# Performance work log

Measured on AMD Instinct MI355X. Metric: run time of the kernel, lower is better.

The kernel has to match this reference:

```python
import jax, jax.numpy as jnp
import numpy as np

DIM = 4096
N_HEADS = 32
N_KV_HEADS = 8
HEAD_DIM = 128
WINDOW = 4096
BATCH = 32
START_POS = 4095


def setup_inputs() -> dict:
    key = jax.random.key(0)
    ks = jax.random.split(key, 8)
    x = jax.random.normal(ks[0], (BATCH, DIM), dtype=jnp.float32)
    wqkv = jax.random.normal(ks[1], (DIM, (N_HEADS + 2 * N_KV_HEADS) * HEAD_DIM), dtype=jnp.float32) * 0.02
    wo = jax.random.normal(ks[2], (N_HEADS * HEAD_DIM, DIM), dtype=jnp.float32) * 0.02
    cos = jax.random.uniform(ks[3], (HEAD_DIM,), dtype=jnp.float32)
    sin = jax.random.uniform(ks[4], (HEAD_DIM,), dtype=jnp.float32)
    cache_k = jax.random.normal(ks[5], (BATCH, N_KV_HEADS, WINDOW, HEAD_DIM), dtype=jnp.float32)
    cache_v = jax.random.normal(ks[6], (BATCH, N_KV_HEADS, WINDOW, HEAD_DIM), dtype=jnp.float32)
    mask = jnp.zeros((BATCH, 1, 1, WINDOW), dtype=jnp.float32)
    return {"x": x, "wqkv": wqkv, "wo": wo, "cos": cos, "sin": sin,
            "cache_k": cache_k, "cache_v": cache_v, "mask": mask,
            "start_pos": START_POS}


def _rotate_half(t):
    t1, t2 = jnp.split(t, 2, axis=-1)
    return jnp.concatenate([-t2, t1], axis=-1)


def _rope(t, cos, sin):
    # t: [..., head_dim]; cos/sin: [head_dim] at the current decode position
    return t * cos + _rotate_half(t) * sin


def reference(x, wqkv, wo, cos, sin, cache_k, cache_v, mask, start_pos):
    B, D = x.shape
    KV = cache_k.shape[1]
    Hd = cache_k.shape[3]
    window = cache_k.shape[2]
    H = wo.shape[0] // Hd
    R = H // KV  # GQA repeats
    scale = 1.0 / np.sqrt(Hd)

    # fused QKV projection (matmul_1d + nlp_create_qkv_heads)
    qkv = x @ wqkv  # [B, (H+2*KV)*Hd]
    q = qkv[:, : H * Hd].reshape(B, H, Hd)
    k = qkv[:, H * Hd : (H + KV) * Hd].reshape(B, KV, Hd)
    v = qkv[:, (H + KV) * Hd :].reshape(B, KV, Hd)

    # rotary embedding on q and k at current position
    q = _rope(q, cos, sin)
    k = _rope(k, cos, sin)

    # sliding-window KV cache update at current_pos
    cur = start_pos % window  # python int
    cache_k = cache_k.at[:, :, cur].set(k)
    cache_v = cache_v.at[:, :, cur].set(v)

    # unpad to padded_layer_past_len = min(nearest_32(start_pos+1), window)
    padded_len = min(((start_pos + 1 + 31) // 32) * 32, window)
    keys = cache_k[:, :, :padded_len]   # [B, KV, T, Hd]
    values = cache_v[:, :, :padded_len]

    # grouped-query attention: q -> [B, KV, R, Hd]
    qg = q.reshape(B, KV, R, Hd)
    scores = jnp.einsum("bgrd,bgtd->bgrt", qg, keys) * scale  # [B, KV, R, T]
    scores = scores + mask[:, :, :, :padded_len]  # broadcast over kv-heads/repeats
    attn = jax.nn.softmax(scores, axis=-1)
    out = jnp.einsum("bgrt,bgtd->bgrd", attn, values)  # [B, KV, R, Hd]

    # concat heads + output projection
    out = out.reshape(B, H * Hd)
    return out @ wo  # [B, D]
```

## Files before the change

kernel.cpp:

```cpp
#include <hip/hip_runtime.h>
#include <math.h>

#define DIM 4096
#define NH 32
#define NKV 8
#define HD 128
#define WINDOW 4096
#define BATCH 32
#define QKV_N 6144
#define ATTN_SCALE 0.08838834764831845f
#define WCHUNK 128
#define NCW 32
#define SLICES 16

__device__ __forceinline__ float4 f4max(float4 a, float4 b) {
  return make_float4(fmaxf(a.x, b.x), fmaxf(a.y, b.y), fmaxf(a.z, b.z), fmaxf(a.w, b.w));
}
__device__ __forceinline__ float4 f4add(float4 a, float4 b) {
  return make_float4(a.x + b.x, a.y + b.y, a.z + b.z, a.w + b.w);
}
__device__ __forceinline__ void fma4(float4& a, float4 x, float4 y) {
  a.x = fmaf(x.x, y.x, a.x); a.y = fmaf(x.y, y.y, a.y);
  a.z = fmaf(x.z, y.z, a.z); a.w = fmaf(x.w, y.w, a.w);
}
__device__ __forceinline__ void fma4s(float4& a, float s, float4 v) {
  a.x = fmaf(s, v.x, a.x); a.y = fmaf(s, v.y, a.y);
  a.z = fmaf(s, v.z, a.z); a.w = fmaf(s, v.w, a.w);
}
__device__ __forceinline__ float4 wred_max(float4 v) {
#pragma unroll
  for (int o = 1; o < 64; o <<= 1) {
    v.x = fmaxf(v.x, __shfl_xor(v.x, o));
    v.y = fmaxf(v.y, __shfl_xor(v.y, o));
    v.z = fmaxf(v.z, __shfl_xor(v.z, o));
    v.w = fmaxf(v.w, __shfl_xor(v.w, o));
  }
  return v;
}
__device__ __forceinline__ float4 wred_add(float4 v) {
#pragma unroll
  for (int o = 1; o < 64; o <<= 1) {
    v.x += __shfl_xor(v.x, o);
    v.y += __shfl_xor(v.y, o);
    v.z += __shfl_xor(v.z, o);
    v.w += __shfl_xor(v.w, o);
  }
  return v;
}
__device__ __forceinline__ void xor32_add(float4& v) {
  v.x += __shfl_xor(v.x, 32);
  v.y += __shfl_xor(v.y, 32);
  v.z += __shfl_xor(v.z, 32);
  v.w += __shfl_xor(v.w, 32);
}

template<int N, int K, int NS>
__global__ __launch_bounds__(256)
void gemm_part(const float* __restrict__ x, const float* __restrict__ w,
               float* __restrict__ part) {
  const int t = threadIdx.x;
  const int c0 = blockIdx.x * 64 + (t & 15) * 4;
  const int r0 = (t >> 4) * 2;
  const int kn = K / NS;
  const int ks = blockIdx.y * kn;

  float a00 = 0.f, a01 = 0.f, a02 = 0.f, a03 = 0.f;
  float a10 = 0.f, a11 = 0.f, a12 = 0.f, a13 = 0.f;

  const float* xr0 = x + (size_t)r0 * K;
  const float* xr1 = xr0 + K;
  const float* wp = w + (size_t)ks * N + c0;

  for (int k = ks; k < ks + kn; k += 4) {
    float4 xa = *(const float4*)(xr0 + k);
    float4 xb = *(const float4*)(xr1 + k);
    float xav[4] = {xa.x, xa.y, xa.z, xa.w};
    float xbv[4] = {xb.x, xb.y, xb.z, xb.w};
#pragma unroll
    for (int kk = 0; kk < 4; ++kk) {
      float4 wv = *(const float4*)(wp);
      wp += N;
      a00 = fmaf(xav[kk], wv.x, a00);
      a01 = fmaf(xav[kk], wv.y, a01);
      a02 = fmaf(xav[kk], wv.z, a02);
      a03 = fmaf(xav[kk], wv.w, a03);
      a10 = fmaf(xbv[kk], wv.x, a10);
      a11 = fmaf(xbv[kk], wv.y, a11);
      a12 = fmaf(xbv[kk], wv.z, a12);
      a13 = fmaf(xbv[kk], wv.w, a13);
    }
  }
  float* p = part + ((size_t)blockIdx.y * 32 + r0) * N + c0;
  *(float4*)p = make_float4(a00, a01, a02, a03);
  *(float4*)(p + N) = make_float4(a10, a11, a12, a13);
}

__global__ __launch_bounds__(256)
void rope_reduce(const float* __restrict__ part, const float* __restrict__ cosv,
                 const float* __restrict__ sinv, float* __restrict__ q,
                 float* __restrict__ knew, float* __restrict__ vnew) {
  int idx = blockIdx.x * 256 + threadIdx.x;
  int r = idx / 3072;
  int rem = idx - r * 3072;
  int head = rem >> 6;
  int d = rem & 63;
  int c1 = head * 128 + d;
  int c2 = c1 + 64;
  float v1 = 0.f, v2 = 0.f;
#pragma unroll
  for (int s = 0; s < SLICES; ++s) {
    v1 += part[((size_t)s * 32 + r) * QKV_N + c1];
    v2 += part[((size_t)s * 32 + r) * QKV_N + c2];
  }
  if (head < NH + NKV) {
    float c_lo = cosv[d], c_hi = cosv[d + 64];
    float s_lo = sinv[d], s_hi = sinv[d + 64];
    float o1 = v1 * c_lo - v2 * s_lo;
    float o2 = v2 * c_hi + v1 * s_hi;
    if (head < NH) {
      q[((size_t)r * NH + head) * HD + d] = o1;
      q[((size_t)r * NH + head) * HD + d + 64] = o2;
    } else {
      int g = head - NH;
      knew[((size_t)r * NKV + g) * HD + d] = o1;
      knew[((size_t)r * NKV + g) * HD + d + 64] = o2;
    }
  } else {
    int g = head - NH - NKV;
    vnew[((size_t)r * NKV + g) * HD + d] = v1;
    vnew[((size_t)r * NKV + g) * HD + d + 64] = v2;
  }
}

__global__ __launch_bounds__(256, 5)
void attn_wave(const float* __restrict__ q, const float* __restrict__ knew,
               const float* __restrict__ vnew, const float* __restrict__ cache_k,
               const float* __restrict__ cache_v, const float* __restrict__ mask,
               const int* __restrict__ start_pos_p,
               float* __restrict__ pvp, float* __restrict__ msp) {
  const int bg = blockIdx.x;
  const int b = bg >> 3;
  const int w = threadIdx.x >> 6;
  const int lane = threadIdx.x & 63;
  const int c = blockIdx.y * 4 + w;
  const int sp = start_pos_p[0];
  const int cur = sp & (WINDOW - 1);
  int plen = ((sp + 1 + 31) >> 5) << 5;
  if (plen > WINDOW) plen = WINDOW;
  const int t0 = c * WCHUNK;
  const int tend = min(t0 + WCHUNK, plen);

  const size_t pidx = ((size_t)c * 256 + bg) * 4;
  float* pvb = pvp + pidx * HD;
  float* msb = msp + pidx * 2;

  __shared__ __align__(16) float q_s[4][4 * HD];
  __shared__ __align__(16) float s_s[4][WCHUNK][4];

  if (t0 >= plen) {
    if (lane < 8) msb[lane] = (lane & 1) ? 0.f : -1e30f;
    for (int i = lane; i < 4 * HD; i += 64) pvb[i] = 0.f;
    return;
  }

  {
    const float* qsrc = q + ((size_t)b * NH + (bg & 7) * 4) * HD;
    float4 v0 = *(const float4*)(qsrc + lane * 8);
    float4 v1 = *(const float4*)(qsrc + lane * 8 + 4);
    *(float4*)(&q_s[w][lane * 8]) = v0;
    *(float4*)(&q_s[w][lane * 8 + 4]) = v1;
  }

  const float* kbase = cache_k + (size_t)bg * WINDOW * HD;
  const float* vbase = cache_v + (size_t)bg * WINDOW * HD;
  const float* krow_new = knew + (size_t)bg * HD;
  const float* vrow_new = vnew + (size_t)bg * HD;

  {
    const int p0 = lane >> 2;
    const int dl = lane & 3;
    for (int tt = t0 + p0; tt < t0 + WCHUNK; tt += 16) {
      if (tt < tend) {
        const float* krow = (tt == cur) ? krow_new : (kbase + (size_t)tt * HD);
        float4 a0 = {0,0,0,0}, a1 = {0,0,0,0}, a2 = {0,0,0,0}, a3 = {0,0,0,0};
#pragma unroll
        for (int j = 0; j < 8; ++j) {
          const int f = dl + 4 * j;
          float4 kv = *(const float4*)(krow + 4 * f);
          fma4(a0, kv, *(const float4*)(&q_s[w][0 * HD + 4 * f]));
          fma4(a1, kv, *(const float4*)(&q_s[w][1 * HD + 4 * f]));
          fma4(a2, kv, *(const float4*)(&q_s[w][2 * HD + 4 * f]));
          fma4(a3, kv, *(const float4*)(&q_s[w][3 * HD + 4 * f]));
        }
        float s0 = a0.x + a0.y + a0.z + a0.w;
        float s1 = a1.x + a1.y + a1.z + a1.w;
        float s2 = a2.x + a2.y + a2.z + a2.w;
        float s3 = a3.x + a3.y + a3.z + a3.w;
        s0 += __shfl_xor(s0, 1); s0 += __shfl_xor(s0, 2);
        s1 += __shfl_xor(s1, 1); s1 += __shfl_xor(s1, 2);
        s2 += __shfl_xor(s2, 1); s2 += __shfl_xor(s2, 2);
        s3 += __shfl_xor(s3, 1); s3 += __shfl_xor(s3, 2);
        float sv = (dl == 0) ? s0 : (dl == 1) ? s1 : (dl == 2) ? s2 : s3;
        s_s[w][tt - t0][dl] = sv * ATTN_SCALE + mask[(size_t)b * WINDOW + tt];
      } else {
        s_s[w][tt - t0][dl] = -1e30f;
      }
    }
  }

  float4 r0 = *(const float4*)(s_s[w][lane]);
  float4 r1 = *(const float4*)(s_s[w][lane + 64]);
  float4 mx = wred_max(f4max(r0, r1));
  float4 e0, e1;
  e0.x = __expf(r0.x - mx.x); e0.y = __expf(r0.y - mx.y);
  e0.z = __expf(r0.z - mx.z); e0.w = __expf(r0.w - mx.w);
  e1.x = __expf(r1.x - mx.x); e1.y = __expf(r1.y - mx.y);
  e1.z = __expf(r1.z - mx.z); e1.w = __expf(r1.w - mx.w);
  *(float4*)(s_s[w][lane]) = e0;
  *(float4*)(s_s[w][lane + 64]) = e1;
  float4 sm = wred_add(f4add(e0, e1));
  if (lane == 0) {
    msb[0] = mx.x; msb[1] = sm.x;
    msb[2] = mx.y; msb[3] = sm.y;
    msb[4] = mx.z; msb[5] = sm.z;
    msb[6] = mx.w; msb[7] = sm.w;
  }

  {
    const int d4 = lane & 31;
    const int half = lane >> 5;
    float4 a0 = {0,0,0,0}, a1 = {0,0,0,0}, a2 = {0,0,0,0}, a3 = {0,0,0,0};
    for (int tt = t0 + half; tt < tend; tt += 2) {
      const float* vrow = (tt == cur) ? vrow_new : (vbase + (size_t)tt * HD);
      float4 vv = *(const float4*)(vrow + 4 * d4);
      float4 p = *(const float4*)(s_s[w][tt - t0]);
      fma4s(a0, p.x, vv);
      fma4s(a1, p.y, vv);
      fma4s(a2, p.z, vv);
      fma4s(a3, p.w, vv);
    }
    xor32_add(a0); xor32_add(a1); xor32_add(a2); xor32_add(a3);
    if (half == 0) {
      *(float4*)(&pvb[0 * HD + 4 * d4]) = a0;
      *(float4*)(&pvb[1 * HD + 4 * d4]) = a1;
      *(float4*)(&pvb[2 * HD + 4 * d4]) = a2;
      *(float4*)(&pvb[3 * HD + 4 * d4]) = a3;
    }
  }
}

__global__ __launch_bounds__(256)
void attn_combine(const float* __restrict__ pvp, const float* __restrict__ msp,
                  float* __restrict__ attn_out) {
  int idx = blockIdx.x * 256 + threadIdx.x;
  int b = idx >> 12;
  int rem = idx & 4095;
  int hf = rem >> 7;
  int d = rem & 127;
  int g = hf >> 2, hh = hf & 3;
  int bg = b * 8 + g;
  float M = -1e30f, den = 0.f, num = 0.f;
#pragma unroll 4
  for (int c = 0; c < NCW; ++c) {
    size_t base = ((size_t)c * 256 + bg) * 4 + hh;
    float m = msp[base * 2];
    float s = msp[base * 2 + 1];
    float p = pvp[base * HD + d];
    float Mn = fmaxf(M, m);
    float so = __expf(M - Mn);
    float sn = __expf(m - Mn);
    den = den * so + s * sn;
    num = num * so + p * sn;
    M = Mn;
  }
  attn_out[idx] = num / den;
}

__global__ __launch_bounds__(256)
void reduce_out(const float* __restrict__ part, float* __restrict__ out) {
  int idx = blockIdx.x * 256 + threadIdx.x;
  float s = 0.f;
#pragma unroll
  for (int sl = 0; sl < SLICES; ++sl) s += part[(size_t)sl * 32 * DIM + idx];
  out[idx] = s;
}

extern "C" void kernel_launch(void* const* d_in, const int* in_sizes, int n_in,
                              void* d_out, int out_size, void* d_ws, size_t ws_size,
                              hipStream_t stream) {
  const float* x       = (const float*)d_in[0];
  const float* wqkv    = (const float*)d_in[1];
  const float* wo      = (const float*)d_in[2];
  const float* cosv    = (const float*)d_in[3];
  const float* sinv    = (const float*)d_in[4];
  const float* cache_k = (const float*)d_in[5];
  const float* cache_v = (const float*)d_in[6];
  const float* mask    = (const float*)d_in[7];
  const int*   start_p = (const int*)d_in[8];
  float* ws = (float*)d_ws;

  float* part     = ws;
  float* q        = ws + 3145728;
  float* knew     = q + 131072;
  float* vnew     = knew + 32768;
  float* attn_out = vnew + 32768;
  float* pvp      = attn_out + 131072;
  float* msp      = pvp + 4194304;
  float* out      = (float*)d_out;

  gemm_part<QKV_N, DIM, SLICES><<<dim3(QKV_N / 64, SLICES), 256, 0, stream>>>(x, wqkv, part);
  rope_reduce<<<384, 256, 0, stream>>>(part, cosv, sinv, q, knew, vnew);
  attn_wave<<<dim3(BATCH * NKV, NCW / 4), 256, 0, stream>>>(q, knew, vnew, cache_k,
                                                            cache_v, mask, start_p,
                                                            pvp, msp);
  attn_combine<<<512, 256, 0, stream>>>(pvp, msp, attn_out);
  gemm_part<DIM, DIM, SLICES><<<dim3(DIM / 64, SLICES), 256, 0, stream>>>(attn_out, wo, part);
  reduce_out<<<512, 256, 0, stream>>>(part, out);
}
```

Before: 368.6 us.

## Retile GEMMs with 8-row register blocking and double attention chunk size

Replaces the split-K GEMM with a version where each thread accumulates eight rows over a 256-column strip and a 128-deep K slice, with 32 slices instead of 16. This reuses each weight load across eight batch rows instead of two. The attention kernel now processes 256-token chunks (16 per head group), preloads K rows into registers, and uses a flat 1D grid, which halves the partial results the combine step must merge. The trade is more partial-sum traffic in the reductions and possibly lower occupancy from higher register pressure.

Result: faster. 340.1 us (-7.7%).

```diff
diff --git a/kernel.cpp b/kernel.cpp
--- a/kernel.cpp
+++ b/kernel.cpp
@@ -9,9 +9,9 @@
 #define BATCH 32
 #define QKV_N 6144
 #define ATTN_SCALE 0.08838834764831845f
-#define WCHUNK 128
-#define NCW 32
-#define SLICES 16
+#define WCHUNK 256
+#define NCW 16
+#define SLICES 32
 
 __device__ __forceinline__ float4 f4max(float4 a, float4 b) {
   return make_float4(fmaxf(a.x, b.x), fmaxf(a.y, b.y), fmaxf(a.z, b.z), fmaxf(a.w, b.w));
@@ -47,58 +47,51 @@
   }
   return v;
 }
-__device__ __forceinline__ void xor32_add(float4& v) {
-  v.x += __shfl_xor(v.x, 32);
-  v.y += __shfl_xor(v.y, 32);
-  v.z += __shfl_xor(v.z, 32);
-  v.w += __shfl_xor(v.w, 32);
-}
-
-template<int N, int K, int NS>
+
+template<int N>
+__global__ __launch_bounds__(256, 4)
+void k_gemm(const float* __restrict__ x, const float* __restrict__ w,
+            float* __restrict__ part, int nstrip) {
+  const int strip = blockIdx.x % nstrip;
+  const int slice = blockIdx.x / nstrip;
+  const int t = threadIdx.x;
+  const int l = t & 63;
+  const int r0 = (t >> 6) * 8;
+  const int ks = slice * 128;
+  const int c0 = strip * 256;
+
+  float4 acc[8];
+#pragma unroll
+  for (int i = 0; i < 8; ++i) acc[i] = make_float4(0.f, 0.f, 0.f, 0.f);
+
+  const float* wp = w + (size_t)ks * N + c0 + 4 * l;
+  const float* xp = x + (size_t)r0 * DIM + ks;
+
+  for (int k4 = 0; k4 < 32; ++k4) {
+    float4 xr[8];
+#pragma unroll
+    for (int r = 0; r < 8; ++r)
+      xr[r] = *(const float4*)(xp + (size_t)r * DIM + 4 * k4);
+#pragma unroll
+    for (int kk = 0; kk < 4; ++kk) {
+      float4 wv = *(const float4*)wp;
+      wp += N;
+#pragma unroll
+      for (int r = 0; r < 8; ++r) {
+        float xs = (kk == 0) ? xr[r].x : (kk == 1) ? xr[r].y : (kk == 2) ? xr[r].z : xr[r].w;
+        fma4s(acc[r], xs, wv);
+      }
+    }
+  }
+  float* p = part + ((size_t)slice * 32 + r0) * N + c0 + 4 * l;
+#pragma unroll
+  for (int i = 0; i < 8; ++i) *(float4*)(p + (size_t)i * N) = acc[i];
+}
+
 __global__ __launch_bounds__(256)
-void gemm_part(const float* __restrict__ x, const float* __restrict__ w,
-               float* __restrict__ part) {
-  const int t = threadIdx.x;
-  const int c0 = blockIdx.x * 64 + (t & 15) * 4;
-  const int r0 = (t >> 4) * 2;
-  const int kn = K / NS;
-  const int ks = blockIdx.y * kn;
-
-  float a00 = 0.f, a01 = 0.f, a02 = 0.f, a03 = 0.f;
-  float a10 = 0.f, a11 = 0.f, a12 = 0.f, a13 = 0.f;
-
-  const float* xr0 = x + (size_t)r0 * K;
-  const float* xr1 = xr0 + K;
-  const float* wp = w + (size_t)ks * N + c0;
-
-  for (int k = ks; k < ks + kn; k += 4) {
-    float4 xa = *(const float4*)(xr0 + k);
-    float4 xb = *(const float4*)(xr1 + k);
-    float xav[4] = {xa.x, xa.y, xa.z, xa.w};
-    float xbv[4] = {xb.x, xb.y, xb.z, xb.w};
-#pragma unroll
-    for (int kk = 0; kk < 4; ++kk) {
-      float4 wv = *(const float4*)(wp);
-      wp += N;
-      a00 = fmaf(xav[kk], wv.x, a00);
-      a01 = fmaf(xav[kk], wv.y, a01);
-      a02 = fmaf(xav[kk], wv.z, a02);
-      a03 = fmaf(xav[kk], wv.w, a03);
-      a10 = fmaf(xbv[kk], wv.x, a10);
-      a11 = fmaf(xbv[kk], wv.y, a11);
-      a12 = fmaf(xbv[kk], wv.z, a12);
-      a13 = fmaf(xbv[kk], wv.w, a13);
-    }
-  }
-  float* p = part + ((size_t)blockIdx.y * 32 + r0) * N + c0;
-  *(float4*)p = make_float4(a00, a01, a02, a03);
-  *(float4*)(p + N) = make_float4(a10, a11, a12, a13);
-}
-
-__global__ __launch_bounds__(256)
-void rope_reduce(const float* __restrict__ part, const float* __restrict__ cosv,
-                 const float* __restrict__ sinv, float* __restrict__ q,
-                 float* __restrict__ knew, float* __restrict__ vnew) {
+void k_rope(const float* __restrict__ part, const float* __restrict__ cosv,
+            const float* __restrict__ sinv, float* __restrict__ q,
+            float* __restrict__ knew, float* __restrict__ vnew) {
   int idx = blockIdx.x * 256 + threadIdx.x;
   int r = idx / 3072;
   int rem = idx - r * 3072;
@@ -107,7 +100,7 @@
   int c1 = head * 128 + d;
   int c2 = c1 + 64;
   float v1 = 0.f, v2 = 0.f;
-#pragma unroll
+#pragma unroll 8
   for (int s = 0; s < SLICES; ++s) {
     v1 += part[((size_t)s * 32 + r) * QKV_N + c1];
     v2 += part[((size_t)s * 32 + r) * QKV_N + c2];
@@ -132,17 +125,22 @@
   }
 }
 
-__global__ __launch_bounds__(256, 5)
-void attn_wave(const float* __restrict__ q, const float* __restrict__ knew,
-               const float* __restrict__ vnew, const float* __restrict__ cache_k,
-               const float* __restrict__ cache_v, const float* __restrict__ mask,
-               const int* __restrict__ start_pos_p,
-               float* __restrict__ pvp, float* __restrict__ msp) {
-  const int bg = blockIdx.x;
+__global__ __launch_bounds__(256, 4)
+void k_attn(const float* __restrict__ q, const float* __restrict__ knew,
+            const float* __restrict__ vnew, const float* __restrict__ cache_k,
+            const float* __restrict__ cache_v, const float* __restrict__ mask,
+            const int* __restrict__ start_pos_p,
+            float* __restrict__ pvp, float* __restrict__ msp) {
+  __shared__ __align__(16) float q_s_all[4][4 * HD];
+  __shared__ __align__(16) float s_s_all[4][WCHUNK * 4];
+  const int t = threadIdx.x;
+  const int w = t >> 6, lane = t & 63;
+  float* q_s = q_s_all[w];
+  float* s_s = s_s_all[w];
+  const int gw = blockIdx.x * 4 + w;
+  const int bg = gw & 255;
+  const int c = gw >> 8;
   const int b = bg >> 3;
-  const int w = threadIdx.x >> 6;
-  const int lane = threadIdx.x & 63;
-  const int c = blockIdx.y * 4 + w;
   const int sp = start_pos_p[0];
   const int cur = sp & (WINDOW - 1);
   int plen = ((sp + 1 + 31) >> 5) << 5;
@@ -154,9 +152,6 @@
   float* pvb = pvp + pidx * HD;
   float* msb = msp + pidx * 2;
 
-  __shared__ __align__(16) float q_s[4][4 * HD];
-  __shared__ __align__(16) float s_s[4][WCHUNK][4];
-
   if (t0 >= plen) {
     if (lane < 8) msb[lane] = (lane & 1) ? 0.f : -1e30f;
     for (int i = lane; i < 4 * HD; i += 64) pvb[i] = 0.f;
@@ -165,10 +160,8 @@
 
   {
     const float* qsrc = q + ((size_t)b * NH + (bg & 7) * 4) * HD;
-    float4 v0 = *(const float4*)(qsrc + lane * 8);
-    float4 v1 = *(const float4*)(qsrc + lane * 8 + 4);
-    *(float4*)(&q_s[w][lane * 8]) = v0;
-    *(float4*)(&q_s[w][lane * 8 + 4]) = v1;
+    *(float4*)(&q_s[lane * 8]) = *(const float4*)(qsrc + lane * 8);
+    *(float4*)(&q_s[lane * 8 + 4]) = *(const float4*)(qsrc + lane * 8 + 4);
   }
 
   const float* kbase = cache_k + (size_t)bg * WINDOW * HD;
@@ -182,15 +175,18 @@
     for (int tt = t0 + p0; tt < t0 + WCHUNK; tt += 16) {
       if (tt < tend) {
         const float* krow = (tt == cur) ? krow_new : (kbase + (size_t)tt * HD);
+        float4 kreg[8];
+#pragma unroll
+        for (int j = 0; j < 8; ++j)
+          kreg[j] = *(const float4*)(krow + 4 * (dl + 4 * j));
         float4 a0 = {0,0,0,0}, a1 = {0,0,0,0}, a2 = {0,0,0,0}, a3 = {0,0,0,0};
 #pragma unroll
         for (int j = 0; j < 8; ++j) {
           const int f = dl + 4 * j;
-          float4 kv = *(const float4*)(krow + 4 * f);
-          fma4(a0, kv, *(const float4*)(&q_s[w][0 * HD + 4 * f]));
-          fma4(a1, kv, *(const float4*)(&q_s[w][1 * HD + 4 * f]));
-          fma4(a2, kv, *(const float4*)(&q_s[w][2 * HD + 4 * f]));
-          fma4(a3, kv, *(const float4*)(&q_s[w][3 * HD + 4 * f]));
+          fma4(a0, kreg[j], *(const float4*)(&q_s[0 * HD + 4 * f]));
+          fma4(a1, kreg[j], *(const float4*)(&q_s[1 * HD + 4 * f]));
+          fma4(a2, kreg[j], *(const float4*)(&q_s[2 * HD + 4 * f]));
+          fma4(a3, kreg[j], *(const float4*)(&q_s[3 * HD + 4 * f]));
         }
         float s0 = a0.x + a0.y + a0.z + a0.w;
         float s1 = a1.x + a1.y + a1.z + a1.w;
@@ -201,24 +197,32 @@
         s2 += __shfl_xor(s2, 1); s2 += __shfl_xor(s2, 2);
         s3 += __shfl_xor(s3, 1); s3 += __shfl_xor(s3, 2);
         float sv = (dl == 0) ? s0 : (dl == 1) ? s1 : (dl == 2) ? s2 : s3;
-        s_s[w][tt - t0][dl] = sv * ATTN_SCALE + mask[(size_t)b * WINDOW + tt];
+        s_s[(tt - t0) * 4 + dl] = sv * ATTN_SCALE + mask[(size_t)b * WINDOW + tt];
       } else {
-        s_s[w][tt - t0][dl] = -1e30f;
+        s_s[(tt - t0) * 4 + dl] = -1e30f;
       }
     }
   }
 
-  float4 r0 = *(const float4*)(s_s[w][lane]);
-  float4 r1 = *(const float4*)(s_s[w][lane + 64]);
-  float4 mx = wred_max(f4max(r0, r1));
-  float4 e0, e1;
-  e0.x = __expf(r0.x - mx.x); e0.y = __expf(r0.y - mx.y);
-  e0.z = __expf(r0.z - mx.z); e0.w = __expf(r0.w - mx.w);
-  e1.x = __expf(r1.x - mx.x); e1.y = __expf(r1.y - mx.y);
-  e1.z = __expf(r1.z - mx.z); e1.w = __expf(r1.w - mx.w);
-  *(float4*)(s_s[w][lane]) = e0;
-  *(float4*)(s_s[w][lane + 64]) = e1;
-  float4 sm = wred_add(f4add(e0, e1));
+  float4 r0v = *(const float4*)(&s_s[(lane +   0) * 4]);
+  float4 r1v = *(const float4*)(&s_s[(lane +  64) * 4]);
+  float4 r2v = *(const float4*)(&s_s[(lane + 128) * 4]);
+  float4 r3v = *(const float4*)(&s_s[(lane + 192) * 4]);
+  float4 mx = wred_max(f4max(f4max(r0v, r1v), f4max(r2v, r3v)));
+  float4 e0, e1, e2, e3;
+  e0.x = __expf(r0v.x - mx.x); e0.y = __expf(r0v.y - mx.y);
+  e0.z = __expf(r0v.z - mx.z); e0.w = __expf(r0v.w - mx.w);
+  e1.x = __expf(r1v.x - mx.x); e1.y = __expf(r1v.y - mx.y);
+  e1.z = __expf(r1v.z - mx.z); e1.w = __expf(r1v.w - mx.w);
+  e2.x = __expf(r2v.x - mx.x); e2.y = __expf(r2v.y - mx.y);
+  e2.z = __expf(r2v.z - mx.z); e2.w = __expf(r2v.w - mx.w);
+  e3.x = __expf(r3v.x - mx.x); e3.y = __expf(r3v.y - mx.y);
+  e3.z = __expf(r3v.z - mx.z); e3.w = __expf(r3v.w - mx.w);
+  *(float4*)(&s_s[(lane +   0) * 4]) = e0;
+  *(float4*)(&s_s[(lane +  64) * 4]) = e1;
+  *(float4*)(&s_s[(lane + 128) * 4]) = e2;
+  *(float4*)(&s_s[(lane + 192) * 4]) = e3;
+  float4 sm = wred_add(f4add(f4add(e0, e1), f4add(e2, e3)));
   if (lane == 0) {
     msb[0] = mx.x; msb[1] = sm.x;
     msb[2] = mx.y; msb[3] = sm.y;
@@ -230,16 +234,24 @@
     const int d4 = lane & 31;
     const int half = lane >> 5;
     float4 a0 = {0,0,0,0}, a1 = {0,0,0,0}, a2 = {0,0,0,0}, a3 = {0,0,0,0};
+#pragma unroll 4
     for (int tt = t0 + half; tt < tend; tt += 2) {
       const float* vrow = (tt == cur) ? vrow_new : (vbase + (size_t)tt * HD);
       float4 vv = *(const float4*)(vrow + 4 * d4);
-      float4 p = *(const float4*)(s_s[w][tt - t0]);
+      float4 p = *(const float4*)(&s_s[(tt - t0) * 4]);
       fma4s(a0, p.x, vv);
       fma4s(a1, p.y, vv);
       fma4s(a2, p.z, vv);
       fma4s(a3, p.w, vv);
     }
-    xor32_add(a0); xor32_add(a1); xor32_add(a2); xor32_add(a3);
+    a0.x += __shfl_xor(a0.x, 32); a0.y += __shfl_xor(a0.y, 32);
+    a0.z += __shfl_xor(a0.z, 32); a0.w += __shfl_xor(a0.w, 32);
+    a1.x += __shfl_xor(a1.x, 32); a1.y += __shfl_xor(a1.y, 32);
+    a1.z += __shfl_xor(a1.z, 32); a1.w += __shfl_xor(a1.w, 32);
+    a2.x += __shfl_xor(a2.x, 32); a2.y += __shfl_xor(a2.y, 32);
+    a2.z += __shfl_xor(a2.z, 32); a2.w += __shfl_xor(a2.w, 32);
+    a3.x += __shfl_xor(a3.x, 32); a3.y += __shfl_xor(a3.y, 32);
+    a3.z += __shfl_xor(a3.z, 32); a3.w += __shfl_xor(a3.w, 32);
     if (half == 0) {
       *(float4*)(&pvb[0 * HD + 4 * d4]) = a0;
       *(float4*)(&pvb[1 * HD + 4 * d4]) = a1;
@@ -250,8 +262,8 @@
 }
 
 __global__ __launch_bounds__(256)
-void attn_combine(const float* __restrict__ pvp, const float* __restrict__ msp,
-                  float* __restrict__ attn_out) {
+void k_combine(const float* __restrict__ pvp, const float* __restrict__ msp,
+               float* __restrict__ attn_out) {
   int idx = blockIdx.x * 256 + threadIdx.x;
   int b = idx >> 12;
   int rem = idx & 4095;
@@ -277,11 +289,11 @@
 }
 
 __global__ __launch_bounds__(256)
-void reduce_out(const float* __restrict__ part, float* __restrict__ out) {
+void k_reduce(const float* __restrict__ part, float* __restrict__ out) {
   int idx = blockIdx.x * 256 + threadIdx.x;
   float s = 0.f;
-#pragma unroll
-  for (int sl = 0; sl < SLICES; ++sl) s += part[(size_t)sl * 32 * DIM + idx];
+#pragma unroll 8
+  for (int sl = 0; sl < SLICES; ++sl) s += part[(size_t)sl * BATCH * DIM + idx];
   out[idx] = s;
 }
 
@@ -299,21 +311,21 @@
   const int*   start_p = (const int*)d_in[8];
   float* ws = (float*)d_ws;
 
-  float* part     = ws;
-  float* q        = ws + 3145728;
+  float* partA    = ws;
+  float* q        = ws + 6291456;
   float* knew     = q + 131072;
   float* vnew     = knew + 32768;
   float* attn_out = vnew + 32768;
   float* pvp      = attn_out + 131072;
-  float* msp      = pvp + 4194304;
+  float* msp      = pvp + 2097152;
+  float* partE    = msp + 16384;
   float* out      = (float*)d_out;
 
-  gemm_part<QKV_N, DIM, SLICES><<<dim3(QKV_N / 64, SLICES), 256, 0, stream>>>(x, wqkv, part);
-  rope_reduce<<<384, 256, 0, stream>>>(part, cosv, sinv, q, knew, vnew);
-  attn_wave<<<dim3(BATCH * NKV, NCW / 4), 256, 0, stream>>>(q, knew, vnew, cache_k,
-                                                            cache_v, mask, start_p,
-                                                            pvp, msp);
-  attn_combine<<<512, 256, 0, stream>>>(pvp, msp, attn_out);
-  gemm_part<DIM, DIM, SLICES><<<dim3(DIM / 64, SLICES), 256, 0, stream>>>(attn_out, wo, part);
-  reduce_out<<<512, 256, 0, stream>>>(part, out);
-}
+  k_gemm<QKV_N><<<24 * SLICES, 256, 0, stream>>>(x, wqkv, partA, 24);
+  k_rope<<<384, 256, 0, stream>>>(partA, cosv, sinv, q, knew, vnew);
+  k_attn<<<(256 * NCW) / 4, 256, 0, stream>>>(q, knew, vnew, cache_k, cache_v,
+                                              mask, start_p, pvp, msp);
+  k_combine<<<512, 256, 0, stream>>>(pvp, msp, attn_out);
+  k_gemm<DIM><<<16 * SLICES, 256, 0, stream>>>(attn_out, wo, partE, 16);
+  k_reduce<<<512, 256, 0, stream>>>(partE, out);
+}
```
